# Kernel tuning notes

Measured on AMD Instinct MI355X. Metric: run time of the kernel, lower is better.

## Reference

```python
import jax, jax.numpy as jnp
import numpy as np

# Deterministic stand-ins for the torch RNG draws in the original forward
# (rot sampled from {0,40,...,320}, shifts from [-20,20], flips from {2,3}).
ROT_DEG = 40.0          # rotations[1]
SHIFTS = (5, -7)        # roll shifts on (H, W)
FLIP_DIMS = (2, 3)      # flip W and D dims (torch.arange(2,4) both selected)


def _rotate_nn_maps(H, W, deg):
    """Nearest-neighbor inverse-rotation index maps for an HxW grid
    (matches torchvision rotate: nearest interp, expand=False, fill=0)."""
    theta = jnp.deg2rad(jnp.float32(deg))
    cy = (H - 1) / 2.0
    cx = (W - 1) / 2.0
    i = jnp.arange(H, dtype=jnp.float32)[:, None] - cy  # [H,1]
    j = jnp.arange(W, dtype=jnp.float32)[None, :] - cx  # [1,W]
    c, s = jnp.cos(theta), jnp.sin(theta)
    # inverse rotation: map each output pixel back to its source location
    src_i = c * i + s * j + cy
    src_j = -s * i + c * j + cx
    si = jnp.round(src_i).astype(jnp.int32)
    sj = jnp.round(src_j).astype(jnp.int32)
    valid = (si >= 0) & (si < H) & (sj >= 0) & (sj < W)
    return jnp.clip(si, 0, H - 1), jnp.clip(sj, 0, W - 1), valid


def setup_inputs() -> dict:
    key = jax.random.key(0)
    features = jax.random.normal(key, (16, 128, 128, 8, 16), dtype=jnp.float32)
    return {"features": features}


def reference(features):
    # features: [B, H, W, D, F]; one fused gather rotates the (H, W) plane for
    # every (sample, depth, feature) simultaneously, replacing the original
    # per-(sample, feature) Python rotate() loop.
    B, H, W, D, F = features.shape
    si, sj, valid = _rotate_nn_maps(H, W, ROT_DEG)
    rotated = jnp.where(valid[None, :, :, None, None],
                        features[:, si, sj, :, :], 0.0)  # [B,H,W,D,F]
    rolled = jnp.roll(rotated, SHIFTS, axis=(1, 2))
    flipped = jnp.flip(rolled, axis=FLIP_DIMS)
    return flipped
```

## Files before the change

kernel.cpp:

```cpp
#include <hip/hip_runtime.h>
#include <math.h>

#define BB 16
#define HH 128
#define WW 128
#define DD 8
#define FF 16


__global__ __launch_bounds__(256) void aug_kernel(const float4* __restrict__ in,
                                                  float4* __restrict__ out,
                                                  int n_vec4) {
    int tid = blockIdx.x * blockDim.x + threadIdx.x;
    if (tid >= n_vec4) return;

    int t  = tid;
    int f4 = t & 3;   t >>= 2;
    int d  = t & 7;   t >>= 3;
    int w  = t & 127; t >>= 7;
    int h  = t & 127; t >>= 7;
    int b  = t;

    int i = (h + 123) & 127;
    int j = (134 - w) & 127;

    const double c = 0.76604444311897803;
    const double s = 0.64278760968653933;
    const double cy = 63.5, cx = 63.5;
    double di = (double)i - cy;
    double dj = (double)j - cx;
    double src_i = c * di + s * dj + cy;
    double src_j = -s * di + c * dj + cx;
    int si = (int)rint(src_i);
    int sj = (int)rint(src_j);
    bool valid = (si >= 0) & (si < HH) & (sj >= 0) & (sj < WW);

    float4 v = make_float4(0.f, 0.f, 0.f, 0.f);
    if (valid) {
        int dd = 7 - d;
        long long src = ((((long long)b * HH + si) * WW + sj) * DD + dd) * 4 + f4;
        v = in[src];
    }
    out[tid] = v;
}

extern "C" void kernel_launch(void* const* d_in, const int* in_sizes, int n_in,
                              void* d_out, int out_size, void* d_ws, size_t ws_size,
                              hipStream_t stream) {
    const float4* in = (const float4*)d_in[0];
    float4* out = (float4*)d_out;
    int n_vec4 = out_size / 4;
    int block = 256;
    int grid = (n_vec4 + block - 1) / block;
    aug_kernel<<<grid, block, 0, stream>>>(in, out, n_vec4);
}
```

Baseline: 221.0 us.

## Loop over batch per thread to amortize index math and use nontemporal stores

```diff
diff --git a/kernel.cpp b/kernel.cpp
--- a/kernel.cpp
+++ b/kernel.cpp
@@ -8,18 +8,15 @@
 #define FF 16
 
 
-__global__ __launch_bounds__(256) void aug_kernel(const float4* __restrict__ in,
-                                                  float4* __restrict__ out,
-                                                  int n_vec4) {
-    int tid = blockIdx.x * blockDim.x + threadIdx.x;
-    if (tid >= n_vec4) return;
+typedef float floatx4 __attribute__((ext_vector_type(4)));
 
-    int t  = tid;
+__global__ __launch_bounds__(256) void aug_kernel(const floatx4* __restrict__ in,
+                                                  floatx4* __restrict__ out) {
+    int t = blockIdx.x * blockDim.x + threadIdx.x;
     int f4 = t & 3;   t >>= 2;
     int d  = t & 7;   t >>= 3;
     int w  = t & 127; t >>= 7;
-    int h  = t & 127; t >>= 7;
-    int b  = t;
+    int h  = t;
 
     int i = (h + 123) & 127;
     int j = (134 - w) & 127;
@@ -29,28 +26,37 @@
     const double cy = 63.5, cx = 63.5;
     double di = (double)i - cy;
     double dj = (double)j - cx;
-    double src_i = c * di + s * dj + cy;
-    double src_j = -s * di + c * dj + cx;
-    int si = (int)rint(src_i);
-    int sj = (int)rint(src_j);
+    int si = (int)rint(c * di + s * dj + cy);
+    int sj = (int)rint(-s * di + c * dj + cx);
     bool valid = (si >= 0) & (si < HH) & (sj >= 0) & (sj < WW);
 
-    float4 v = make_float4(0.f, 0.f, 0.f, 0.f);
+    const int STRIDE = HH * WW * DD * (FF / 4);
+    int out0 = ((h * WW + w) * DD + d) * 4 + f4;
+
     if (valid) {
         int dd = 7 - d;
-        long long src = ((((long long)b * HH + si) * WW + sj) * DD + dd) * 4 + f4;
-        v = in[src];
+        int src0 = ((si * WW + sj) * DD + dd) * 4 + f4;
+        #pragma unroll
+        for (int b = 0; b < BB; ++b) {
+            floatx4 v = in[src0 + b * STRIDE];
+            __builtin_nontemporal_store(v, &out[out0 + b * STRIDE]);
+        }
+    } else {
+        floatx4 z = (floatx4)(0.f);
+        #pragma unroll
+        for (int b = 0; b < BB; ++b) {
+            __builtin_nontemporal_store(z, &out[out0 + b * STRIDE]);
+        }
     }
-    out[tid] = v;
 }
 
 extern "C" void kernel_launch(void* const* d_in, const int* in_sizes, int n_in,
                               void* d_out, int out_size, void* d_ws, size_t ws_size,
                               hipStream_t stream) {
-    const float4* in = (const float4*)d_in[0];
-    float4* out = (float4*)d_out;
-    int n_vec4 = out_size / 4;
+    const floatx4* in = (const floatx4*)d_in[0];
+    floatx4* out = (floatx4*)d_out;
+    int n_threads = HH * WW * DD * (FF / 4);
     int block = 256;
-    int grid = (n_vec4 + block - 1) / block;
-    aug_kernel<<<grid, block, 0, stream>>>(in, out, n_vec4);
+    int grid = n_threads / block;
+    aug_kernel<<<grid, block, 0, stream>>>(in, out);
 }
```

After: 235.4 us. +6.5%, slower.
